# Kernel optimization log

Measured on AMD Instinct MI355X. Metric: run time of the kernel, lower is better.

The kernel has to match this reference:

```python
import jax, jax.numpy as jnp
import numpy as np

NUM_HEADS = 32
NUM_KV_HEADS = 8
HEAD_DIM = 128
SCALE = 1.0 / np.sqrt(128.0)
B = 8          # num sequences
LQ = 1024 // 8 # new (query) tokens per sequence
PAGE_SIZE = 16


def setup_inputs() -> dict:
    key = jax.random.key(0)
    ks = jax.random.split(key, 5)
    q = jax.random.normal(ks[0], (B * LQ, NUM_HEADS * HEAD_DIM), dtype=jnp.float32)
    k = jax.random.normal(ks[1], (B * LQ, NUM_KV_HEADS * HEAD_DIM), dtype=jnp.float32)
    v = jax.random.normal(ks[2], (B * LQ, NUM_KV_HEADS * HEAD_DIM), dtype=jnp.float32)
    k_cache = jax.random.normal(ks[3], (1024, PAGE_SIZE, NUM_KV_HEADS, HEAD_DIM), dtype=jnp.float32)
    v_cache = jax.random.normal(ks[4], (1024, PAGE_SIZE, NUM_KV_HEADS, HEAD_DIM), dtype=jnp.float32)
    page_tables = jnp.arange(8 * 128, dtype=jnp.int64).reshape(8, 128)  # distinct pages per seq
    return {"q": q, "k": k, "v": v, "k_cache": k_cache, "v_cache": v_cache,
            "page_tables": page_tables, "ctx_len": 2048, "block_size": 32}


def reference(q, k, v, k_cache, v_cache, page_tables, ctx_len, block_size):
    nh, nkvh, hd = NUM_HEADS, NUM_KV_HEADS, HEAD_DIM
    group = nh // nkvh
    # split flat token dim into [B, Lq]
    qs = q.reshape(B, LQ, nh, hd)
    k_new = k.reshape(B, LQ, nkvh, hd)
    v_new = v.reshape(B, LQ, nkvh, hd)
    # paged gather of cached context: [B, n_pages, P, nkvh, hd] -> [B, ctx_len, nkvh, hd]
    k_ctx = k_cache[page_tables].reshape(B, ctx_len, nkvh, hd)
    v_ctx = v_cache[page_tables].reshape(B, ctx_len, nkvh, hd)
    k_full = jnp.concatenate([k_ctx, k_new], axis=1)  # [B, ctx_len+Lq, nkvh, hd]
    v_full = jnp.concatenate([v_ctx, v_new], axis=1)
    # GQA: repeat kv heads to match query heads (repeat_interleave over head dim)
    k_rep = jnp.repeat(k_full, group, axis=2)  # [B, K, nh, hd]
    v_rep = jnp.repeat(v_full, group, axis=2)
    scores = jnp.einsum('bqhd,bkhd->bhqk', qs, k_rep) * SCALE  # [B, nh, Lq, K]
    # diffusion block-causal mask over the new-token region; cache region fully visible
    qi = jnp.arange(LQ)
    abs_q = ctx_len + qi
    abs_k_new = ctx_len + jnp.arange(LQ)
    block_ends = (abs_q // block_size + 1) * block_size
    new_mask = abs_k_new[None, :] < block_ends[:, None]            # [Lq, Lq]
    cache_mask = jnp.ones((LQ, ctx_len), dtype=bool)
    mask = jnp.concatenate([cache_mask, new_mask], axis=1)         # [Lq, ctx_len+Lq]
    neg = jnp.finfo(scores.dtype).min
    scores = jnp.where(mask[None, None, :, :], scores, neg)
    probs = jax.nn.softmax(scores, axis=-1)
    out = jnp.einsum('bhqk,bkhd->bqhd', probs, v_rep)  # [B, Lq, nh, hd]
    return out.reshape(B * LQ, nh * hd).astype(q.dtype)
```

## Files before the change

kernel.cpp:

```cpp
#include <hip/hip_runtime.h>
#include <math.h>

#define NH 32
#define NKVH 8
#define GRP 4
#define HD 128
#define LQB 128
#define B_SEQ 8
#define PTSTRIDE 128
#define KVROW (NKVH * HD)
#define QK_SCALE 0.08838834764831845f
#define LOG2E 1.4426950408889634f
#define DEFER_THR 8.0f
#define NROWS (B_SEQ * LQB * NH)

typedef __attribute__((ext_vector_type(8))) __bf16 bf16x8;
typedef __attribute__((ext_vector_type(4))) __bf16 bf16x4;
typedef __attribute__((ext_vector_type(4))) float f32x4;

#define KS_BYTES 8192
#define VT_STRIDE 80
#define VT_BYTES 10240
#define KS_OFF(b) ((b) * KS_BYTES)
#define VT_OFF(b) (2 * KS_BYTES + (b) * VT_BYTES)

static __device__ __forceinline__ bf16x8 cvt8s(const float* __restrict__ p, float s) {
    const f32x4 a = *reinterpret_cast<const f32x4*>(p);
    const f32x4 b = *reinterpret_cast<const f32x4*>(p + 4);
    bf16x8 r;
    r[0] = (__bf16)(a[0] * s); r[1] = (__bf16)(a[1] * s);
    r[2] = (__bf16)(a[2] * s); r[3] = (__bf16)(a[3] * s);
    r[4] = (__bf16)(b[0] * s); r[5] = (__bf16)(b[1] * s);
    r[6] = (__bf16)(b[2] * s); r[7] = (__bf16)(b[3] * s);
    return r;
}

template<int NSPLIT>
__global__ __launch_bounds__(256, 4)
void attn_fwd(const float* __restrict__ Q,
              const float* __restrict__ Kn,
              const float* __restrict__ Vn,
              const float* __restrict__ Kc,
              const float* __restrict__ Vc,
              const int* __restrict__ PT,
              const int* __restrict__ CTX,
              float* __restrict__ O,
              float* __restrict__ WA,
              float2* __restrict__ WML)
{
    __shared__ __align__(16) unsigned char smem[2 * KS_BYTES + 2 * VT_BYTES];

    const int ctx  = CTX[0];
    const int tid  = (int)threadIdx.x;
    const int wave = tid >> 6;
    const int lane = tid & 63;
    const int low  = lane & 15;
    const int hi   = lane >> 4;

    const int bid   = (int)blockIdx.x;
    const int kvh   = bid & 7;
    const int b     = (bid >> 3) & 7;
    const int qtile = (bid >> 6) & 7;
    const int sk    = (NSPLIT > 1) ? (bid >> 9) : 0;
    const int head  = kvh * GRP + wave;
    const int q0    = qtile * 16;

    const int qtok = b * LQB + q0 + low;
    const float* qrow = Q + (size_t)qtok * (NH * HD) + head * HD;

    bf16x8 qf[4];
    #pragma unroll
    for (int c = 0; c < 4; ++c) qf[c] = cvt8s(qrow + 32 * c + 8 * hi, QK_SCALE * LOG2E);

    f32x4 acc[8];
    #pragma unroll
    for (int c = 0; c < 8; ++c) acc[c] = (f32x4){0.f, 0.f, 0.f, 0.f};
    float mrun = -1e30f, lrun = 0.f;

    const int vis  = ctx + (((q0 >> 5) + 1) << 5);
    const int nt   = vis >> 5;
    const int kbeg = ((nt * sk) / NSPLIT) << 5;
    const int kend = ((nt * (sk + 1)) / NSPLIT) << 5;
    const int nsteps = (kend - kbeg) >> 5;

    const int skey = tid >> 3;
    const int sc8  = tid & 7;
    const int kxr  = (skey & 15) << 4;
    const int vdc  = tid >> 3;
    const int vkq  = tid & 7;

    f32x4 kr[4], vr[4];

    auto issue_loads = [&](int t0) {
        {
            const int tok = t0 + skey;
            const float* src; size_t ro;
            if (tok < ctx) {
                const int pg = PT[b * PTSTRIDE + (tok >> 4)];
                src = Kc; ro = ((size_t)pg * 16 + (tok & 15)) * KVROW + kvh * HD;
            } else {
                src = Kn; ro = (size_t)(b * LQB + tok - ctx) * KVROW + kvh * HD;
            }
            const f32x4* p = reinterpret_cast<const f32x4*>(src + ro + 16 * sc8);
            kr[0] = p[0]; kr[1] = p[1]; kr[2] = p[2]; kr[3] = p[3];
        }
        {
            const int tok0 = t0 + 4 * vkq;
            const float* src; size_t ro;
            if (tok0 < ctx) {
                const int pg = PT[b * PTSTRIDE + (tok0 >> 4)];
                src = Vc; ro = ((size_t)pg * 16 + (tok0 & 15)) * KVROW + kvh * HD;
            } else {
                src = Vn; ro = (size_t)(b * LQB + tok0 - ctx) * KVROW + kvh * HD;
            }
            const float* base = src + ro + 4 * vdc;
            vr[0] = *reinterpret_cast<const f32x4*>(base);
            vr[1] = *reinterpret_cast<const f32x4*>(base + KVROW);
            vr[2] = *reinterpret_cast<const f32x4*>(base + 2 * KVROW);
            vr[3] = *reinterpret_cast<const f32x4*>(base + 3 * KVROW);
        }
    };

    auto write_tile = [&](int buf) {
        unsigned char* ks = smem + KS_OFF(buf) + skey * 256;
        bf16x8 c0w, c1w;
        #pragma unroll
        for (int j = 0; j < 4; ++j) {
            c0w[j] = (__bf16)kr[0][j]; c0w[j + 4] = (__bf16)kr[1][j];
            c1w[j] = (__bf16)kr[2][j]; c1w[j + 4] = (__bf16)kr[3][j];
        }
        *reinterpret_cast<bf16x8*>(ks + ((32 * sc8) ^ kxr))      = c0w;
        *reinterpret_cast<bf16x8*>(ks + ((32 * sc8 + 16) ^ kxr)) = c1w;
        unsigned char* vt = smem + VT_OFF(buf) + 8 * vkq;
        #pragma unroll
        for (int di = 0; di < 4; ++di) {
            bf16x4 w;
            w[0] = (__bf16)vr[0][di]; w[1] = (__bf16)vr[1][di];
            w[2] = (__bf16)vr[2][di]; w[3] = (__bf16)vr[3][di];
            *reinterpret_cast<bf16x4*>(vt + (4 * vdc + di) * VT_STRIDE) = w;
        }
    };

    auto tile_barrier = [&]() {
        asm volatile("s_waitcnt lgkmcnt(0)" ::: "memory");
        __builtin_amdgcn_s_barrier();
    };

    issue_loads(kbeg);
    write_tile(0);
    if (nsteps > 1) issue_loads(kbeg + 32);
    tile_barrier();

    int cur = 0;
    for (int s = 0; s < nsteps; ++s) {
        if (s + 1 < nsteps) write_tile(cur ^ 1);
        if (s + 2 < nsteps) issue_loads(kbeg + ((s + 2) << 5));

        const unsigned char* ks = smem + KS_OFF(cur);
        const unsigned char* vt = smem + VT_OFF(cur);
        const int xr = low << 4;

        f32x4 s0 = (f32x4){0.f, 0.f, 0.f, 0.f};
        f32x4 s1 = (f32x4){0.f, 0.f, 0.f, 0.f};
        #pragma unroll
        for (int c = 0; c < 4; ++c) {
            bf16x8 ka = *reinterpret_cast<const bf16x8*>(ks + low * 256 + ((64 * c + 16 * hi) ^ xr));
            bf16x8 kb = *reinterpret_cast<const bf16x8*>(ks + (16 + low) * 256 + ((64 * c + 16 * hi) ^ xr));
            s0 = __builtin_amdgcn_mfma_f32_16x16x32_bf16(ka, qf[c], s0, 0, 0, 0);
            s1 = __builtin_amdgcn_mfma_f32_16x16x32_bf16(kb, qf[c], s1, 0, 0, 0);
        }

        float pmax = fmaxf(fmaxf(fmaxf(s0[0], s0[1]), fmaxf(s0[2], s0[3])),
                           fmaxf(fmaxf(s1[0], s1[1]), fmaxf(s1[2], s1[3])));

        if (!__all(pmax - mrun <= DEFER_THR)) {
            float pm = fmaxf(pmax, __shfl_xor(pmax, 16));
            pm = fmaxf(pm, __shfl_xor(pm, 32));
            const float mnew = fmaxf(mrun, pm);
            const float corr = exp2f(mrun - mnew);
            mrun = mnew;
            lrun *= corr;
            #pragma unroll
            for (int c = 0; c < 8; ++c) acc[c] *= corr;
        }

        float p[8];
        #pragma unroll
        for (int j = 0; j < 4; ++j) {
            p[j]     = exp2f(s0[j] - mrun);
            p[j + 4] = exp2f(s1[j] - mrun);
        }
        lrun += (((p[0] + p[1]) + (p[2] + p[3])) + ((p[4] + p[5]) + (p[6] + p[7])));

        bf16x8 pf;
        #pragma unroll
        for (int j = 0; j < 8; ++j) pf[j] = (__bf16)p[j];

        #pragma unroll
        for (int c = 0; c < 8; ++c) {
            const unsigned char* vrow = vt + (16 * c + low) * VT_STRIDE + 8 * hi;
            bf16x4 a0 = *reinterpret_cast<const bf16x4*>(vrow);
            bf16x4 a1 = *reinterpret_cast<const bf16x4*>(vrow + 32);
            bf16x8 vf;
            vf[0] = a0[0]; vf[1] = a0[1]; vf[2] = a0[2]; vf[3] = a0[3];
            vf[4] = a1[0]; vf[5] = a1[1]; vf[6] = a1[2]; vf[7] = a1[3];
            acc[c] = __builtin_amdgcn_mfma_f32_16x16x32_bf16(vf, pf, acc[c], 0, 0, 0);
        }

        if (s + 1 < nsteps) tile_barrier();
        cur ^= 1;
    }

    lrun += __shfl_xor(lrun, 16);
    lrun += __shfl_xor(lrun, 32);

    const int r = qtok * NH + head;
    if (NSPLIT > 1) {
        float* oa = WA + ((size_t)sk * NROWS + r) * HD;
        #pragma unroll
        for (int c = 0; c < 8; ++c)
            *reinterpret_cast<f32x4*>(oa + 16 * c + 4 * hi) = acc[c];
        if (hi == 0) WML[sk * NROWS + r] = make_float2(mrun, lrun);
    } else {
        const float inv = 1.0f / lrun;
        float* orow = O + (size_t)r * HD;
        #pragma unroll
        for (int c = 0; c < 8; ++c) {
            f32x4 v = acc[c] * inv;
            *reinterpret_cast<f32x4*>(orow + 16 * c + 4 * hi) = v;
        }
    }
}

template<int NSPLIT>
__global__ __launch_bounds__(256)
void combine(const float* __restrict__ WA, const float2* __restrict__ WML,
             float* __restrict__ O)
{
    const int idx = (int)blockIdx.x * 256 + (int)threadIdx.x;
    const int r  = idx >> 5;
    const int dq = idx & 31;
    float2 ml[NSPLIT];
    float M = -1e30f;
    #pragma unroll
    for (int s = 0; s < NSPLIT; ++s) { ml[s] = WML[s * NROWS + r]; M = fmaxf(M, ml[s].x); }
    float e[NSPLIT];
    float den = 0.f;
    #pragma unroll
    for (int s = 0; s < NSPLIT; ++s) { e[s] = exp2f(ml[s].x - M); den += ml[s].y * e[s]; }
    const float inv = 1.0f / den;
    f32x4 o = (f32x4){0.f, 0.f, 0.f, 0.f};
    #pragma unroll
    for (int s = 0; s < NSPLIT; ++s) {
        const f32x4 a = *reinterpret_cast<const f32x4*>(WA + ((size_t)s * NROWS + r) * HD + 4 * dq);
        o += a * e[s];
    }
    o *= inv;
    *reinterpret_cast<f32x4*>(O + (size_t)r * HD + 4 * dq) = o;
}

extern "C" void kernel_launch(void* const* d_in, const int* in_sizes, int n_in,
                              void* d_out, int out_size, void* d_ws, size_t ws_size,
                              hipStream_t stream) {
    const float* q  = (const float*)d_in[0];
    const float* k  = (const float*)d_in[1];
    const float* v  = (const float*)d_in[2];
    const float* kc = (const float*)d_in[3];
    const float* vc = (const float*)d_in[4];
    const int*   pt = (const int*)d_in[5];
    const int*   cx = (const int*)d_in[6];
    float* out = (float*)d_out;

    const size_t wa2   = (size_t)2 * NROWS * HD * sizeof(float);
    const size_t need2 = wa2 + (size_t)2 * NROWS * sizeof(float2);

    if (ws_size >= need2) {
        float*  wa  = (float*)d_ws;
        float2* wml = (float2*)((char*)d_ws + wa2);
        attn_fwd<2><<<dim3(1024), dim3(256), 0, stream>>>(q, k, v, kc, vc, pt, cx, out, wa, wml);
        combine<2><<<dim3(NROWS * 32 / 256), dim3(256), 0, stream>>>(wa, wml, out);
    } else {
        attn_fwd<1><<<dim3(512), dim3(256), 0, stream>>>(q, k, v, kc, vc, pt, cx, out,
                                                         nullptr, nullptr);
    }
}
```

Before: 270.7 us.

## Switch attention to 32x32x16 MFMA with 32-query tiles and 3-way KV split

Moves the attention kernel from 16x16x32 to 32x32x16 bf16 MFMA tiles, so each wave handles 32 query rows. Each K/V tile loaded into shared memory is therefore reused by twice as many queries, halving redundant K/V global loads and conversions. The P operand is rebuilt through cross-half lane shuffles. The KV split rises to 3 (768 blocks), occupancy is lowered to 3, and every path now goes through the workspace and combine kernel. The costs are a larger register footprint, per-row correction shuffles on rescale, and scalar (non-vector) workspace stores.

```diff
diff --git a/kernel.cpp b/kernel.cpp
--- a/kernel.cpp
+++ b/kernel.cpp
@@ -14,15 +14,16 @@
 #define DEFER_THR 8.0f
 #define NROWS (B_SEQ * LQB * NH)
 
-typedef __attribute__((ext_vector_type(8))) __bf16 bf16x8;
-typedef __attribute__((ext_vector_type(4))) __bf16 bf16x4;
-typedef __attribute__((ext_vector_type(4))) float f32x4;
+typedef __attribute__((ext_vector_type(8)))  __bf16 bf16x8;
+typedef __attribute__((ext_vector_type(4)))  __bf16 bf16x4;
+typedef __attribute__((ext_vector_type(4)))  float  f32x4;
+typedef __attribute__((ext_vector_type(16))) float  f32x16;
 
 #define KS_BYTES 8192
 #define VT_STRIDE 80
 #define VT_BYTES 10240
-#define KS_OFF(b) ((b) * KS_BYTES)
-#define VT_OFF(b) (2 * KS_BYTES + (b) * VT_BYTES)
+#define KS_OFF(bu) ((bu) * KS_BYTES)
+#define VT_OFF(bu) (2 * KS_BYTES + (bu) * VT_BYTES)
 
 static __device__ __forceinline__ bf16x8 cvt8s(const float* __restrict__ p, float s) {
     const f32x4 a = *reinterpret_cast<const f32x4*>(p);
@@ -36,7 +37,7 @@
 }
 
 template<int NSPLIT>
-__global__ __launch_bounds__(256, 4)
+__global__ __launch_bounds__(256, 3)
 void attn_fwd(const float* __restrict__ Q,
               const float* __restrict__ Kn,
               const float* __restrict__ Vn,
@@ -44,7 +45,6 @@
               const float* __restrict__ Vc,
               const int* __restrict__ PT,
               const int* __restrict__ CTX,
-              float* __restrict__ O,
               float* __restrict__ WA,
               float2* __restrict__ WML)
 {
@@ -54,30 +54,30 @@
     const int tid  = (int)threadIdx.x;
     const int wave = tid >> 6;
     const int lane = tid & 63;
-    const int low  = lane & 15;
-    const int hi   = lane >> 4;
+    const int c31  = lane & 31;
+    const int hl   = lane >> 5;
 
     const int bid   = (int)blockIdx.x;
     const int kvh   = bid & 7;
     const int b     = (bid >> 3) & 7;
-    const int qtile = (bid >> 6) & 7;
-    const int sk    = (NSPLIT > 1) ? (bid >> 9) : 0;
+    const int qtile = (bid >> 6) & 3;
+    const int sk    = (NSPLIT > 1) ? (bid >> 8) : 0;
     const int head  = kvh * GRP + wave;
-    const int q0    = qtile * 16;
-
-    const int qtok = b * LQB + q0 + low;
-    const float* qrow = Q + (size_t)qtok * (NH * HD) + head * HD;
-
-    bf16x8 qf[4];
-    #pragma unroll
-    for (int c = 0; c < 4; ++c) qf[c] = cvt8s(qrow + 32 * c + 8 * hi, QK_SCALE * LOG2E);
-
-    f32x4 acc[8];
-    #pragma unroll
-    for (int c = 0; c < 8; ++c) acc[c] = (f32x4){0.f, 0.f, 0.f, 0.f};
-    float mrun = -1e30f, lrun = 0.f;
-
-    const int vis  = ctx + (((q0 >> 5) + 1) << 5);
+    const int q0    = qtile * 32;
+
+    const float* qrow = Q + (size_t)(b * LQB + q0 + c31) * (NH * HD) + head * HD;
+    bf16x8 qf[8];
+    #pragma unroll
+    for (int c = 0; c < 8; ++c) qf[c] = cvt8s(qrow + 16 * c + 8 * hl, QK_SCALE * LOG2E);
+
+    f32x16 acc[4];
+    #pragma unroll
+    for (int g = 0; g < 4; ++g)
+        #pragma unroll
+        for (int r = 0; r < 16; ++r) acc[g][r] = 0.f;
+    float mrun = -1e30f, lsum = 0.f;
+
+    const int vis  = ctx + q0 + 32;
     const int nt   = vis >> 5;
     const int kbeg = ((nt * sk) / NSPLIT) << 5;
     const int kend = ((nt * (sk + 1)) / NSPLIT) << 5;
@@ -121,8 +121,8 @@
         }
     };
 
-    auto write_tile = [&](int buf) {
-        unsigned char* ks = smem + KS_OFF(buf) + skey * 256;
+    auto write_tile = [&](int bu) {
+        unsigned char* ks = smem + KS_OFF(bu) + skey * 256;
         bf16x8 c0w, c1w;
         #pragma unroll
         for (int j = 0; j < 4; ++j) {
@@ -131,7 +131,7 @@
         }
         *reinterpret_cast<bf16x8*>(ks + ((32 * sc8) ^ kxr))      = c0w;
         *reinterpret_cast<bf16x8*>(ks + ((32 * sc8 + 16) ^ kxr)) = c1w;
-        unsigned char* vt = smem + VT_OFF(buf) + 8 * vkq;
+        unsigned char* vt = smem + VT_OFF(bu) + 8 * vkq;
         #pragma unroll
         for (int di = 0; di < 4; ++di) {
             bf16x4 w;
@@ -158,78 +158,85 @@
 
         const unsigned char* ks = smem + KS_OFF(cur);
         const unsigned char* vt = smem + VT_OFF(cur);
-        const int xr = low << 4;
-
-        f32x4 s0 = (f32x4){0.f, 0.f, 0.f, 0.f};
-        f32x4 s1 = (f32x4){0.f, 0.f, 0.f, 0.f};
-        #pragma unroll
-        for (int c = 0; c < 4; ++c) {
-            bf16x8 ka = *reinterpret_cast<const bf16x8*>(ks + low * 256 + ((64 * c + 16 * hi) ^ xr));
-            bf16x8 kb = *reinterpret_cast<const bf16x8*>(ks + (16 + low) * 256 + ((64 * c + 16 * hi) ^ xr));
-            s0 = __builtin_amdgcn_mfma_f32_16x16x32_bf16(ka, qf[c], s0, 0, 0, 0);
-            s1 = __builtin_amdgcn_mfma_f32_16x16x32_bf16(kb, qf[c], s1, 0, 0, 0);
-        }
-
-        float pmax = fmaxf(fmaxf(fmaxf(s0[0], s0[1]), fmaxf(s0[2], s0[3])),
-                           fmaxf(fmaxf(s1[0], s1[1]), fmaxf(s1[2], s1[3])));
-
-        if (!__all(pmax - mrun <= DEFER_THR)) {
-            float pm = fmaxf(pmax, __shfl_xor(pmax, 16));
-            pm = fmaxf(pm, __shfl_xor(pm, 32));
+        const int xr = (c31 & 15) << 4;
+
+        f32x16 sc;
+        #pragma unroll
+        for (int r = 0; r < 16; ++r) sc[r] = 0.f;
+        #pragma unroll
+        for (int c = 0; c < 8; ++c) {
+            bf16x8 kf = *reinterpret_cast<const bf16x8*>(
+                ks + c31 * 256 + ((((2 * c + hl) << 4)) ^ xr));
+            sc = __builtin_amdgcn_mfma_f32_32x32x16_bf16(kf, qf[c], sc, 0, 0, 0);
+        }
+
+        float pm = sc[0];
+        #pragma unroll
+        for (int r = 1; r < 16; ++r) pm = fmaxf(pm, sc[r]);
+        pm = fmaxf(pm, __shfl_xor(pm, 32));
+
+        if (!__all(pm - mrun <= DEFER_THR)) {
             const float mnew = fmaxf(mrun, pm);
             const float corr = exp2f(mrun - mnew);
             mrun = mnew;
-            lrun *= corr;
+            lsum *= corr;
             #pragma unroll
-            for (int c = 0; c < 8; ++c) acc[c] *= corr;
-        }
-
-        float p[8];
-        #pragma unroll
-        for (int j = 0; j < 4; ++j) {
-            p[j]     = exp2f(s0[j] - mrun);
-            p[j + 4] = exp2f(s1[j] - mrun);
-        }
-        lrun += (((p[0] + p[1]) + (p[2] + p[3])) + ((p[4] + p[5]) + (p[6] + p[7])));
-
-        bf16x8 pf;
-        #pragma unroll
-        for (int j = 0; j < 8; ++j) pf[j] = (__bf16)p[j];
-
-        #pragma unroll
-        for (int c = 0; c < 8; ++c) {
-            const unsigned char* vrow = vt + (16 * c + low) * VT_STRIDE + 8 * hi;
-            bf16x4 a0 = *reinterpret_cast<const bf16x4*>(vrow);
-            bf16x4 a1 = *reinterpret_cast<const bf16x4*>(vrow + 32);
-            bf16x8 vf;
-            vf[0] = a0[0]; vf[1] = a0[1]; vf[2] = a0[2]; vf[3] = a0[3];
-            vf[4] = a1[0]; vf[5] = a1[1]; vf[6] = a1[2]; vf[7] = a1[3];
-            acc[c] = __builtin_amdgcn_mfma_f32_16x16x32_bf16(vf, pf, acc[c], 0, 0, 0);
+            for (int r = 0; r < 16; ++r) {
+                const int qr = (r & 3) + 8 * (r >> 2) + 4 * hl;
+                const float cr = __shfl(corr, qr);
+                #pragma unroll
+                for (int g = 0; g < 4; ++g) acc[g][r] *= cr;
+            }
+        }
+
+        float p[16];
+        float ss = 0.f;
+        #pragma unroll
+        for (int r = 0; r < 16; ++r) {
+            p[r] = exp2f(sc[r] - mrun);
+            ss += p[r];
+        }
+        lsum += ss;
+
+        #pragma unroll
+        for (int h = 0; h < 2; ++h) {
+            union { bf16x4 h4; uint2 u2; } U, W;
+            #pragma unroll
+            for (int m = 0; m < 4; ++m) {
+                U.h4[m] = (__bf16)p[8 * h + m];
+                W.h4[m] = (__bf16)p[8 * h + 4 + m];
+            }
+            const unsigned sux = __shfl_xor(U.u2.x, 32), suy = __shfl_xor(U.u2.y, 32);
+            const unsigned swx = __shfl_xor(W.u2.x, 32), swy = __shfl_xor(W.u2.y, 32);
+            union { bf16x8 h8; unsigned u[4]; } PF;
+            PF.u[0] = hl ? swx : U.u2.x;
+            PF.u[1] = hl ? swy : U.u2.y;
+            PF.u[2] = hl ? W.u2.x : sux;
+            PF.u[3] = hl ? W.u2.y : suy;
+            #pragma unroll
+            for (int g = 0; g < 4; ++g) {
+                bf16x8 vf = *reinterpret_cast<const bf16x8*>(
+                    vt + (32 * g + c31) * VT_STRIDE + 32 * h + 16 * hl);
+                acc[g] = __builtin_amdgcn_mfma_f32_32x32x16_bf16(PF.h8, vf, acc[g], 0, 0, 0);
+            }
         }
 
         if (s + 1 < nsteps) tile_barrier();
         cur ^= 1;
     }
 
-    lrun += __shfl_xor(lrun, 16);
-    lrun += __shfl_xor(lrun, 32);
-
-    const int r = qtok * NH + head;
-    if (NSPLIT > 1) {
-        float* oa = WA + ((size_t)sk * NROWS + r) * HD;
-        #pragma unroll
-        for (int c = 0; c < 8; ++c)
-            *reinterpret_cast<f32x4*>(oa + 16 * c + 4 * hi) = acc[c];
-        if (hi == 0) WML[sk * NROWS + r] = make_float2(mrun, lrun);
-    } else {
-        const float inv = 1.0f / lrun;
-        float* orow = O + (size_t)r * HD;
-        #pragma unroll
-        for (int c = 0; c < 8; ++c) {
-            f32x4 v = acc[c] * inv;
-            *reinterpret_cast<f32x4*>(orow + 16 * c + 4 * hi) = v;
-        }
-    }
+    lsum += __shfl_xor(lsum, 32);
+
+    #pragma unroll
+    for (int g = 0; g < 4; ++g)
+        #pragma unroll
+        for (int r = 0; r < 16; ++r) {
+            const int qr = (r & 3) + 8 * (r >> 2) + 4 * hl;
+            WA[((size_t)sk * NROWS + (size_t)(b * LQB + q0 + qr) * NH + head) * HD
+               + 32 * g + c31] = acc[g][r];
+        }
+    if (lane < 32)
+        WML[sk * NROWS + (b * LQB + q0 + lane) * NH + head] = make_float2(mrun, lsum);
 }
 
 template<int NSPLIT>
@@ -271,16 +278,23 @@
     const int*   cx = (const int*)d_in[6];
     float* out = (float*)d_out;
 
-    const size_t wa2   = (size_t)2 * NROWS * HD * sizeof(float);
-    const size_t need2 = wa2 + (size_t)2 * NROWS * sizeof(float2);
-
-    if (ws_size >= need2) {
+    const size_t waN = (size_t)NROWS * HD * sizeof(float);
+    const size_t mlN = (size_t)NROWS * sizeof(float2);
+
+    if (ws_size >= 3 * (waN + mlN)) {
         float*  wa  = (float*)d_ws;
-        float2* wml = (float2*)((char*)d_ws + wa2);
-        attn_fwd<2><<<dim3(1024), dim3(256), 0, stream>>>(q, k, v, kc, vc, pt, cx, out, wa, wml);
+        float2* wml = (float2*)((char*)d_ws + 3 * waN);
+        attn_fwd<3><<<dim3(768), dim3(256), 0, stream>>>(q, k, v, kc, vc, pt, cx, wa, wml);
+        combine<3><<<dim3(NROWS * 32 / 256), dim3(256), 0, stream>>>(wa, wml, out);
+    } else if (ws_size >= 2 * (waN + mlN)) {
+        float*  wa  = (float*)d_ws;
+        float2* wml = (float2*)((char*)d_ws + 2 * waN);
+        attn_fwd<2><<<dim3(512), dim3(256), 0, stream>>>(q, k, v, kc, vc, pt, cx, wa, wml);
         combine<2><<<dim3(NROWS * 32 / 256), dim3(256), 0, stream>>>(wa, wml, out);
     } else {
-        attn_fwd<1><<<dim3(512), dim3(256), 0, stream>>>(q, k, v, kc, vc, pt, cx, out,
-                                                         nullptr, nullptr);
+        float*  wa  = (float*)d_ws;
+        float2* wml = (float2*)((char*)d_ws + waN);
+        attn_fwd<1><<<dim3(256), dim3(256), 0, stream>>>(q, k, v, kc, vc, pt, cx, wa, wml);
+        combine<1><<<dim3(NROWS * 32 / 256), dim3(256), 0, stream>>>(wa, wml, out);
     }
 }
```

Result: slower. 316.9 us (+17.1%).
